# Kernel tuning notes

Hardware: AMD Instinct MI355X
Metric: run time of the kernel (lower is better)

## Reference

```python
import jax, jax.numpy as jnp
import numpy as np

# ---- Hash-grid configuration (matches init_kwargs / torch-ngp HashEncoder) ----
L = 16            # num_levels
D = 2             # level_dim
BASE = 16         # base_resolution
DESIRED = 2048    # desired_resolution
MAXP = 2 ** 19    # 2**log2_hashmap_size
DIVIDE = 1.5

S = np.exp2(np.log2(DESIRED / BASE) / (L - 1))          # per-level scale ~1.3819
RES = np.ceil(BASE * S ** np.arange(L)).astype(np.int64)  # [L] grid resolutions
_sizes = np.minimum(MAXP, (RES + 1) ** 3)
SIZES = (np.ceil(_sizes / 8) * 8).astype(np.int64)       # aligned to 8, per torch-ngp
OFFSETS = np.concatenate([[0], np.cumsum(SIZES)[:-1]])
TOTAL = int(SIZES.sum())  # 6119864
DENSE = (RES + 1) ** 3 <= SIZES                          # levels small enough for direct index
PRIMES = (1, 2654435761, 805459861)


def hash_encode(x01, table):
    """x01: [N,3] in [0,1]; table: [TOTAL, D]. Returns [N, L*D]."""
    N = x01.shape[0]
    scale = jnp.asarray(BASE * S ** np.arange(L) - 1.0, jnp.float32)   # [L]
    pos = x01[:, None, :] * scale[None, :, None] + 0.5                 # [N,L,3]
    pg_f = jnp.floor(pos)
    frac = pos - pg_f                                                  # [N,L,3]
    pg = pg_f.astype(jnp.uint32)

    res1 = jnp.asarray(RES + 1, jnp.uint32)        # [L]
    sizes = jnp.asarray(SIZES, jnp.uint32)         # [L]
    offs = jnp.asarray(OFFSETS, jnp.int32)         # [L]
    dense = jnp.asarray(DENSE)                     # [L] bool

    feat = jnp.zeros((N, L, D), x01.dtype)
    for c in range(8):  # 8 trilinear corners (fixed small loop)
        bit = np.array([(c >> 0) & 1, (c >> 1) & 1, (c >> 2) & 1])
        cg = pg + jnp.asarray(bit, jnp.uint32)                         # [N,L,3]
        w = jnp.prod(jnp.where(jnp.asarray(bit.astype(bool)), frac, 1.0 - frac), axis=-1)  # [N,L]
        idx_dense = cg[..., 0] + cg[..., 1] * res1 + cg[..., 2] * res1 * res1
        h = (cg[..., 0] * jnp.uint32(PRIMES[0])) ^ (cg[..., 1] * jnp.uint32(PRIMES[1])) ^ (cg[..., 2] * jnp.uint32(PRIMES[2]))
        idx = jnp.where(dense[None, :], idx_dense % sizes, h % sizes)  # [N,L]
        gidx = idx.astype(jnp.int32) + offs[None, :]                   # global table index
        feat = feat + w[..., None] * table[gidx]                       # gather + lerp accumulate
    return feat.reshape(N, L * D)


def setup_inputs() -> dict:
    key = jax.random.key(0)
    ks = jax.random.split(key, 10)
    N = 524288
    x = jax.random.uniform(ks[0], (N, 3), jnp.float32)                # coords in [0,1)
    table = jax.random.uniform(ks[1], (TOTAL, D), jnp.float32, -1e-4, 1e-4)
    def lin(k, fi, fo):
        return jax.random.normal(k, (fi, fo), jnp.float32) / np.sqrt(fi)
    return {
        'x': x, 'table': table,
        'w1': lin(ks[2], 32, 256), 'b1': jnp.zeros((256,), jnp.float32),
        'w2': lin(ks[3], 256, 256), 'b2': jnp.zeros((256,), jnp.float32),
        'w3': lin(ks[4], 256, 256), 'b3': jnp.zeros((256,), jnp.float32),
        'w4': lin(ks[5], 256, 3), 'b4': jnp.zeros((3,), jnp.float32),
    }


def reference(x, table, w1, b1, w2, b2, w3, b3, w4, b4):
    feat = hash_encode(x / DIVIDE, table)                 # [N,32]
    h = jax.nn.relu(feat @ w1 + b1)
    h = jax.nn.relu(h @ w2 + b2)
    h = jax.nn.relu(h @ w3 + b3)
    rgb = jax.nn.sigmoid(h @ w4 + b4)                     # [N,3]
    return rgb
```

## Files before the change

kernel.cpp:

```cpp
#include <hip/hip_runtime.h>
#include <hip/hip_bf16.h>
#include <math.h>

#define NTHREADS 256
#define BR 64

typedef __attribute__((ext_vector_type(8))) short   s16x8;
typedef __attribute__((ext_vector_type(8))) __bf16  bf16x8;
typedef __attribute__((ext_vector_type(4))) float   f32x4;
typedef __attribute__((ext_vector_type(2))) float   f32x2;

__device__ __constant__ float c_scale[16] = {
    15.0f,        21.110607f,  29.554930f,  41.224254f,
    57.350239f,   79.634946f,  110.430473f, 152.987205f,
    211.796890f,  293.066769f, 405.374657f, 560.574388f,
    775.046906f,  1071.429232f, 1481.003616f, 2047.0f
};
__device__ __constant__ unsigned c_off[16] = {
    0u,        4920u,     18744u,    51512u,
    136696u,   352696u,   876984u,   1401272u,
    1925560u,  2449848u,  2974136u,  3498424u,
    4022712u,  4547000u,  5071288u,  5595576u
};
__device__ __constant__ unsigned c_res1[16] = {
    17u, 24u, 32u, 44u, 60u, 0u,0u,0u,0u,0u,0u,0u,0u,0u,0u,0u
};

#define TBL_SCALE     8192.0f
#define TBL_SCALE_INV (1.0f/8192.0f)

__device__ inline unsigned short f2bf(float f) {
    unsigned u = __builtin_bit_cast(unsigned, f);
    u += 0x7FFFu + ((u >> 16) & 1u);
    return (unsigned short)(u >> 16);
}
__device__ inline float bf2f(unsigned short h) {
    unsigned u = ((unsigned)h) << 16;
    return __builtin_bit_cast(float, u);
}
__device__ inline unsigned cvtpk(float lo, float hi) {
    unsigned r;
    asm("v_cvt_pk_bf16_f32 %0, %1, %2" : "=v"(r) : "v"(lo), "v"(hi));
    return r;
}
__device__ inline f32x4 mfma_bf16(s16x8 a, s16x8 b, f32x4 c) {
    return __builtin_amdgcn_mfma_f32_16x16x32_bf16(
        __builtin_bit_cast(bf16x8, a), __builtin_bit_cast(bf16x8, b), c, 0, 0, 0);
}

__global__ void convert_w(const float* __restrict__ w1, const float* __restrict__ w2,
                          const float* __restrict__ w3, const float* __restrict__ w4,
                          unsigned short* __restrict__ ws) {
    int t = blockIdx.x * blockDim.x + threadIdx.x;
    if (t < 8192) {
        int col = t >> 5, k = t & 31;
        ws[t] = f2bf(w1[k * 256 + col]);
    } else if (t < 73728) {
        int u = t - 8192; int col = u >> 8, k = u & 255;
        ws[t] = f2bf(w2[k * 256 + col]);
    } else if (t < 139264) {
        int u = t - 73728; int col = u >> 8, k = u & 255;
        ws[t] = f2bf(w3[k * 256 + col]);
    } else if (t < 143360) {
        int u = t - 139264; int ch = u >> 8, k = u & 255;
        ws[t] = (ch < 3) ? f2bf(w4[k * 3 + ch]) : (unsigned short)0;
    }
}

__global__ void convert_table_fp8(const float* __restrict__ t, unsigned short* __restrict__ o, int n) {
    int i = blockIdx.x * blockDim.x + threadIdx.x;
    if (i < n) {
        const float2 v = ((const float2*)t)[i];
        const int pk = __builtin_amdgcn_cvt_pk_fp8_f32(v.x * TBL_SCALE, v.y * TBL_SCALE, 0, false);
        o[i] = (unsigned short)(pk & 0xFFFF);
    }
}

__global__ __launch_bounds__(256)
void encode_kernel(const float* __restrict__ x, const unsigned short* __restrict__ tbf8,
                   uint2* __restrict__ feat2, int N)
{
    const int p  = blockIdx.x * 256 + threadIdx.x;
    const int lp = blockIdx.y;
    if (p >= N) return;

    const float inv = (1.0f / 1.5f);
    const float xc = x[3 * p + 0] * inv;
    const float yc = x[3 * p + 1] * inv;
    const float zc = x[3 * p + 2] * inv;

    unsigned idxa[2][8];
    float rxa[2], rya[2], rza[2];
    #pragma unroll
    for (int s = 0; s < 2; ++s) {
        const int l = lp * 2 + s;
        const float sc = c_scale[l];
        const float px = xc * sc + 0.5f;
        const float py = yc * sc + 0.5f;
        const float pz = zc * sc + 0.5f;
        const float fx = floorf(px), fy = floorf(py), fz = floorf(pz);
        rxa[s] = px - fx; rya[s] = py - fy; rza[s] = pz - fz;
        const unsigned ux = (unsigned)fx, uy = (unsigned)fy, uz = (unsigned)fz;
        const unsigned off = c_off[l];
        const unsigned r1  = c_res1[l];
        const bool dense = (l < 5);
        #pragma unroll
        for (int c = 0; c < 8; ++c) {
            const unsigned cx = ux + (c & 1), cy = uy + ((c >> 1) & 1), cz = uz + ((c >> 2) & 1);
            unsigned idx;
            if (dense) idx = cx + cy * r1 + cz * r1 * r1;
            else       idx = (cx ^ (cy * 2654435761u) ^ (cz * 805459861u)) & 524287u;
            idxa[s][c] = idx + off;
        }
    }

    unsigned short va[2][8];
    #pragma unroll
    for (int s = 0; s < 2; ++s)
        #pragma unroll
        for (int c = 0; c < 8; ++c)
            va[s][c] = tbf8[idxa[s][c]];

    unsigned outv[2];
    #pragma unroll
    for (int s = 0; s < 2; ++s) {
        float ax = 0.0f, ay = 0.0f;
        #pragma unroll
        for (int c = 0; c < 8; ++c) {
            const float wx = (c & 1) ? rxa[s] : (1.0f - rxa[s]);
            const float wy = ((c >> 1) & 1) ? rya[s] : (1.0f - rya[s]);
            const float wz = ((c >> 2) & 1) ? rza[s] : (1.0f - rza[s]);
            const float w = wx * wy * wz;
            const f32x2 tv = __builtin_amdgcn_cvt_pk_f32_fp8((int)va[s][c], false);
            ax = fmaf(w, tv[0], ax);
            ay = fmaf(w, tv[1], ay);
        }
        outv[s] = cvtpk(ax * TBL_SCALE_INV, ay * TBL_SCALE_INV);
    }
    feat2[(size_t)lp * N + p] = make_uint2(outv[0], outv[1]);
}

__global__ __launch_bounds__(NTHREADS, 3)
void mlp_kernel(const uint2* __restrict__ feat2,
                const unsigned short* __restrict__ wt,
                const float* __restrict__ b1, const float* __restrict__ b2,
                const float* __restrict__ b3, const float* __restrict__ b4,
                float* __restrict__ out, int N)
{
    __shared__ unsigned short sA[BR * 256];
    char* sAb = (char*)sA;

    const int tid = threadIdx.x;
    const int p0  = blockIdx.x * BR;
    if (p0 >= N) return;

    #pragma unroll
    for (int it = 0; it < 2; ++it) {
        const int t  = it * NTHREADS + tid;
        const int lp = t >> 6;
        const int p  = t & 63;
        const uint2 v = feat2[(size_t)lp * N + p0 + p];
        *reinterpret_cast<uint2*>(
            sAb + p * 512 + (((unsigned)(lp * 8)) ^ ((unsigned)((p & 7) << 4)))) = v;
    }
    __syncthreads();

    const int lane = tid & 63;
    const int wid  = tid >> 6;
    const int rowb = wid * 64;
    const int arow = lane & 15;
    const int kgrp = lane >> 4;
    const int bcol = lane & 15;

    f32x4 acc[4][4];

    auto epilogue = [&](const float* __restrict__ bias) {
        #pragma unroll
        for (int rt = 0; rt < 4; ++rt) {
            const int f0 = rowb + rt * 16 + kgrp * 4;
            const float4 bv = *reinterpret_cast<const float4*>(bias + f0);
            #pragma unroll
            for (int ct = 0; ct < 4; ++ct) {
                const int p = ct * 16 + bcol;
                const float v0 = fmaxf(acc[rt][ct][0] + bv.x, 0.0f);
                const float v1 = fmaxf(acc[rt][ct][1] + bv.y, 0.0f);
                const float v2 = fmaxf(acc[rt][ct][2] + bv.z, 0.0f);
                const float v3 = fmaxf(acc[rt][ct][3] + bv.w, 0.0f);
                uint2 pk;
                pk.x = cvtpk(v0, v1);
                pk.y = cvtpk(v2, v3);
                *reinterpret_cast<uint2*>(
                    sAb + p * 512 + (((unsigned)(2 * f0)) ^ ((unsigned)((p & 7) << 4)))) = pk;
            }
        }
    };

    {
        #pragma unroll
        for (int rt = 0; rt < 4; ++rt)
            #pragma unroll
            for (int ct = 0; ct < 4; ++ct) acc[rt][ct] = f32x4{0.f, 0.f, 0.f, 0.f};

        s16x8 wfr[4];
        #pragma unroll
        for (int rt = 0; rt < 4; ++rt)
            wfr[rt] = *reinterpret_cast<const s16x8*>(wt + (rowb + rt * 16 + arow) * 32 + kgrp * 8);
        #pragma unroll
        for (int ct = 0; ct < 4; ++ct) {
            const int p = ct * 16 + bcol;
            const s16x8 bfr = *reinterpret_cast<const s16x8*>(
                sAb + p * 512 + (((unsigned)(kgrp * 16)) ^ ((unsigned)((p & 7) << 4))));
            #pragma unroll
            for (int rt = 0; rt < 4; ++rt)
                acc[rt][ct] = mfma_bf16(wfr[rt], bfr, acc[rt][ct]);
        }
        __syncthreads();
        epilogue(b1);
        __syncthreads();
    }

    #pragma unroll 1
    for (int layer = 0; layer < 2; ++layer) {
        const unsigned short* __restrict__ W = wt + 8192 + (layer << 16);
        #pragma unroll
        for (int rt = 0; rt < 4; ++rt)
            #pragma unroll
            for (int ct = 0; ct < 4; ++ct) acc[rt][ct] = f32x4{0.f, 0.f, 0.f, 0.f};

        for (int ks = 0; ks < 8; ++ks) {
            s16x8 wfr[4];
            #pragma unroll
            for (int rt = 0; rt < 4; ++rt)
                wfr[rt] = *reinterpret_cast<const s16x8*>(
                    W + (rowb + rt * 16 + arow) * 256 + ks * 32 + kgrp * 8);
            #pragma unroll
            for (int ct = 0; ct < 4; ++ct) {
                const int p = ct * 16 + bcol;
                const s16x8 bfr = *reinterpret_cast<const s16x8*>(
                    sAb + p * 512 + (((unsigned)(ks * 64 + kgrp * 16)) ^ ((unsigned)((p & 7) << 4))));
                #pragma unroll
                for (int rt = 0; rt < 4; ++rt)
                    acc[rt][ct] = mfma_bf16(wfr[rt], bfr, acc[rt][ct]);
            }
        }
        __syncthreads();
        epilogue(layer == 0 ? b2 : b3);
        __syncthreads();
    }

    {
        const unsigned short* __restrict__ W4 = wt + 139264;
        const int p = wid * 16 + bcol;
        f32x4 a4 = f32x4{0.f, 0.f, 0.f, 0.f};
        #pragma unroll
        for (int ks = 0; ks < 8; ++ks) {
            const s16x8 wfr = *reinterpret_cast<const s16x8*>(W4 + arow * 256 + ks * 32 + kgrp * 8);
            const s16x8 bfr = *reinterpret_cast<const s16x8*>(
                sAb + p * 512 + (((unsigned)(ks * 64 + kgrp * 16)) ^ ((unsigned)((p & 7) << 4))));
            a4 = mfma_bf16(wfr, bfr, a4);
        }
        if (kgrp == 0) {
            const int pi = p0 + p;
            if (pi < N) {
                #pragma unroll
                for (int c = 0; c < 3; ++c) {
                    const float z = a4[c] + b4[c];
                    out[pi * 3 + c] = 1.0f / (1.0f + expf(-z));
                }
            }
        }
    }
}

__global__ __launch_bounds__(NTHREADS, 3)
void fused_hashmlp(const float* __restrict__ x, const float* __restrict__ table,
                   const unsigned short* __restrict__ wt,
                   const float* __restrict__ b1, const float* __restrict__ b2,
                   const float* __restrict__ b3,
                   const float* __restrict__ w4, const float* __restrict__ b4,
                   float* __restrict__ out, int N)
{
    __shared__ float sX[BR][3];
    __shared__ unsigned short sA[BR * 256];
    const int tid = threadIdx.x;
    const int p0  = blockIdx.x * BR;
    if (p0 >= N) return;
    char* sAb = (char*)sA;

    if (tid < BR * 3) sX[tid / 3][tid % 3] = x[p0 * 3 + tid];
    __syncthreads();

    #pragma unroll
    for (int it = 0; it < 4; ++it) {
        const int task = it * NTHREADS + tid;
        const int l = task >> 6;
        const int p = task & 63;
        const float sc  = c_scale[l];
        const float inv = (1.0f / 1.5f);
        const float px = sX[p][0] * inv * sc + 0.5f;
        const float py = sX[p][1] * inv * sc + 0.5f;
        const float pz = sX[p][2] * inv * sc + 0.5f;
        const float fx = floorf(px), fy = floorf(py), fz = floorf(pz);
        const float rx = px - fx, ry = py - fy, rz = pz - fz;
        const unsigned ux = (unsigned)fx, uy = (unsigned)fy, uz = (unsigned)fz;
        const unsigned off = c_off[l];
        const unsigned r1  = c_res1[l];
        const bool dense = (l < 5);
        float ax = 0.0f, ay = 0.0f;
        #pragma unroll
        for (int c = 0; c < 8; ++c) {
            const unsigned bx = c & 1, by = (c >> 1) & 1, bz = (c >> 2) & 1;
            const unsigned cx = ux + bx, cy = uy + by, cz = uz + bz;
            const float wx = bx ? rx : (1.0f - rx);
            const float wy = by ? ry : (1.0f - ry);
            const float wz = bz ? rz : (1.0f - rz);
            const float w = wx * wy * wz;
            unsigned idx;
            if (dense) idx = cx + cy * r1 + cz * r1 * r1;
            else       idx = (cx ^ (cy * 2654435761u) ^ (cz * 805459861u)) & 524287u;
            const float2 tv = *reinterpret_cast<const float2*>(table + 2u * (idx + off));
            ax = fmaf(w, tv.x, ax);
            ay = fmaf(w, tv.y, ay);
        }
        const unsigned pack = (unsigned)f2bf(ax) | ((unsigned)f2bf(ay) << 16);
        *reinterpret_cast<unsigned*>(sAb + p * 512 + ((l * 4) ^ ((p & 7) << 4))) = pack;
    }
    __syncthreads();

    const int lane = tid & 63;
    const int wid  = tid >> 6;
    const int rowb = wid * 64;
    const int arow = lane & 15;
    const int kgrp = lane >> 4;
    const int bcol = lane & 15;

    f32x4 acc[4][4];

    auto epilogue = [&](const float* __restrict__ bias) {
        #pragma unroll
        for (int rt = 0; rt < 4; ++rt) {
            const int f0 = rowb + rt * 16 + kgrp * 4;
            const float4 bv = *reinterpret_cast<const float4*>(bias + f0);
            #pragma unroll
            for (int ct = 0; ct < 4; ++ct) {
                const int p = ct * 16 + bcol;
                const float v0 = fmaxf(acc[rt][ct][0] + bv.x, 0.0f);
                const float v1 = fmaxf(acc[rt][ct][1] + bv.y, 0.0f);
                const float v2 = fmaxf(acc[rt][ct][2] + bv.z, 0.0f);
                const float v3 = fmaxf(acc[rt][ct][3] + bv.w, 0.0f);
                uint2 pk;
                pk.x = (unsigned)f2bf(v0) | ((unsigned)f2bf(v1) << 16);
                pk.y = (unsigned)f2bf(v2) | ((unsigned)f2bf(v3) << 16);
                *reinterpret_cast<uint2*>(
                    sAb + p * 512 + (((unsigned)(2 * f0)) ^ ((unsigned)((p & 7) << 4)))) = pk;
            }
        }
    };

    {
        #pragma unroll
        for (int rt = 0; rt < 4; ++rt)
            #pragma unroll
            for (int ct = 0; ct < 4; ++ct) acc[rt][ct] = f32x4{0.f, 0.f, 0.f, 0.f};
        s16x8 wfr[4];
        #pragma unroll
        for (int rt = 0; rt < 4; ++rt)
            wfr[rt] = *reinterpret_cast<const s16x8*>(wt + (rowb + rt * 16 + arow) * 32 + kgrp * 8);
        #pragma unroll
        for (int ct = 0; ct < 4; ++ct) {
            const int p = ct * 16 + bcol;
            const s16x8 bfr = *reinterpret_cast<const s16x8*>(
                sAb + p * 512 + (((unsigned)(kgrp * 16)) ^ ((unsigned)((p & 7) << 4))));
            #pragma unroll
            for (int rt = 0; rt < 4; ++rt)
                acc[rt][ct] = mfma_bf16(wfr[rt], bfr, acc[rt][ct]);
        }
        __syncthreads();
        epilogue(b1);
        __syncthreads();
    }

    #pragma unroll 1
    for (int layer = 0; layer < 2; ++layer) {
        const unsigned short* __restrict__ W = wt + 8192 + (layer << 16);
        #pragma unroll
        for (int rt = 0; rt < 4; ++rt)
            #pragma unroll
            for (int ct = 0; ct < 4; ++ct) acc[rt][ct] = f32x4{0.f, 0.f, 0.f, 0.f};
        for (int ks = 0; ks < 8; ++ks) {
            s16x8 wfr[4];
            #pragma unroll
            for (int rt = 0; rt < 4; ++rt)
                wfr[rt] = *reinterpret_cast<const s16x8*>(
                    W + (rowb + rt * 16 + arow) * 256 + ks * 32 + kgrp * 8);
            #pragma unroll
            for (int ct = 0; ct < 4; ++ct) {
                const int p = ct * 16 + bcol;
                const s16x8 bfr = *reinterpret_cast<const s16x8*>(
                    sAb + p * 512 + (((unsigned)(ks * 64 + kgrp * 16)) ^ ((unsigned)((p & 7) << 4))));
                #pragma unroll
                for (int rt = 0; rt < 4; ++rt)
                    acc[rt][ct] = mfma_bf16(wfr[rt], bfr, acc[rt][ct]);
            }
        }
        __syncthreads();
        epilogue(layer == 0 ? b2 : b3);
        __syncthreads();
    }

    if (tid < BR * 3) {
        const int r = tid / 3;
        const int c = tid - 3 * r;
        float z0 = 0.0f, z1 = 0.0f;
        for (int kb = 0; kb < 32; kb += 2) {
            const s16x8 hv0 = *reinterpret_cast<const s16x8*>(
                sAb + r * 512 + (((unsigned)(kb * 16)) ^ ((unsigned)((r & 7) << 4))));
            const s16x8 hv1 = *reinterpret_cast<const s16x8*>(
                sAb + r * 512 + (((unsigned)((kb + 1) * 16)) ^ ((unsigned)((r & 7) << 4))));
            #pragma unroll
            for (int j = 0; j < 8; ++j) {
                z0 = fmaf(bf2f((unsigned short)hv0[j]), w4[(kb * 8 + j) * 3 + c], z0);
                z1 = fmaf(bf2f((unsigned short)hv1[j]), w4[((kb + 1) * 8 + j) * 3 + c], z1);
            }
        }
        const float z = z0 + z1 + b4[c];
        const int pi = p0 + r;
        if (pi < N) out[pi * 3 + c] = 1.0f / (1.0f + expf(-z));
    }
}

extern "C" void kernel_launch(void* const* d_in, const int* in_sizes, int n_in,
                              void* d_out, int out_size, void* d_ws, size_t ws_size,
                              hipStream_t stream) {
    const float* x     = (const float*)d_in[0];
    const float* table = (const float*)d_in[1];
    const float* w1    = (const float*)d_in[2];
    const float* b1    = (const float*)d_in[3];
    const float* w2    = (const float*)d_in[4];
    const float* b2    = (const float*)d_in[5];
    const float* w3    = (const float*)d_in[6];
    const float* b3    = (const float*)d_in[7];
    const float* w4    = (const float*)d_in[8];
    const float* b4    = (const float*)d_in[9];
    float* out = (float*)d_out;

    const int N = in_sizes[0] / 3;

    const size_t W_ELEMS    = 143360;
    const size_t TOTAL_E    = 6119864;
    const size_t wt_bytes   = W_ELEMS * 2;
    const size_t tbl_bytes  = TOTAL_E * 2;
    const size_t need_bf    = wt_bytes + tbl_bytes;
    const size_t FEAT_BYTES = (size_t)N * 64;
    const size_t need_split = need_bf + FEAT_BYTES;

    unsigned short* wsw  = (unsigned short*)d_ws;
    unsigned short* tbf8 = (unsigned short*)((char*)d_ws + wt_bytes);
    uint2* feat2 = (uint2*)((char*)d_ws + need_bf);

    hipLaunchKernelGGL(convert_w, dim3(560), dim3(256), 0, stream, w1, w2, w3, w4, wsw);

    if (ws_size >= need_split) {
        hipLaunchKernelGGL(convert_table_fp8, dim3((unsigned)((TOTAL_E + 255) / 256)), dim3(256),
                           0, stream, table, tbf8, (int)TOTAL_E);
        hipLaunchKernelGGL(encode_kernel, dim3((N + 255) / 256, 8), dim3(256), 0, stream,
                           x, tbf8, feat2, N);
        hipLaunchKernelGGL(mlp_kernel, dim3((N + BR - 1) / BR), dim3(NTHREADS), 0, stream,
                           feat2, wsw, b1, b2, b3, b4, out, N);
    } else {
        hipLaunchKernelGGL(fused_hashmlp, dim3((N + BR - 1) / BR), dim3(NTHREADS), 0, stream,
                           x, table, wsw, b1, b2, b3, w4, b4, out, N);
    }
}
```

Baseline: 558.9 us.

## Merge x-adjacent hash-grid corner gathers and widen MLP blocks to 128 rows

The encode kernel now pairs the two x-neighbour corners of each trilinear cell. When their table indices fall in the same aligned 32-bit word, both come from a single 4-byte load; otherwise it falls back to a separate 2-byte gather for the second corner. Dense levels and hashed levels with an even x coordinate qualify, so this should cut the number of random memory transactions. The MLP kernel moves from 256 threads and 64 rows per block to 512 threads and 128 rows, with pairs of waves sharing weight rows. That doubles LDS per block to 64 KB, which may limit how many blocks fit on a CU.

```diff
diff --git a/kernel.cpp b/kernel.cpp
--- a/kernel.cpp
+++ b/kernel.cpp
@@ -4,6 +4,8 @@
 
 #define NTHREADS 256
 #define BR 64
+#define MTHREADS 512
+#define MBR 128
 
 typedef __attribute__((ext_vector_type(8))) short   s16x8;
 typedef __attribute__((ext_vector_type(8))) __bf16  bf16x8;
@@ -89,7 +91,7 @@
     const float yc = x[3 * p + 1] * inv;
     const float zc = x[3 * p + 2] * inv;
 
-    unsigned idxa[2][8];
+    unsigned i0a[2][4], i1a[2][4];
     float rxa[2], rya[2], rza[2];
     #pragma unroll
     for (int s = 0; s < 2; ++s) {
@@ -105,69 +107,95 @@
         const unsigned r1  = c_res1[l];
         const bool dense = (l < 5);
         #pragma unroll
-        for (int c = 0; c < 8; ++c) {
-            const unsigned cx = ux + (c & 1), cy = uy + ((c >> 1) & 1), cz = uz + ((c >> 2) & 1);
-            unsigned idx;
-            if (dense) idx = cx + cy * r1 + cz * r1 * r1;
-            else       idx = (cx ^ (cy * 2654435761u) ^ (cz * 805459861u)) & 524287u;
-            idxa[s][c] = idx + off;
-        }
-    }
-
-    unsigned short va[2][8];
+        for (int j = 0; j < 4; ++j) {
+            const unsigned cy = uy + (j & 1), cz = uz + (j >> 1);
+            unsigned i0, i1;
+            if (dense) {
+                i0 = ux + cy * r1 + cz * r1 * r1;
+                i1 = i0 + 1;
+            } else {
+                const unsigned m = (cy * 2654435761u) ^ (cz * 805459861u);
+                i0 = (ux ^ m) & 524287u;
+                i1 = ((ux + 1u) ^ m) & 524287u;
+            }
+            i0a[s][j] = i0 + off;
+            i1a[s][j] = i1 + off;
+        }
+    }
+
+    unsigned da[2][4];
     #pragma unroll
     for (int s = 0; s < 2; ++s)
         #pragma unroll
-        for (int c = 0; c < 8; ++c)
-            va[s][c] = tbf8[idxa[s][c]];
+        for (int j = 0; j < 4; ++j)
+            da[s][j] = *reinterpret_cast<const unsigned*>(tbf8 + (i0a[s][j] & ~1u));
+
+    unsigned short fb[2][4];
+    #pragma unroll
+    for (int s = 0; s < 2; ++s)
+        #pragma unroll
+        for (int j = 0; j < 4; ++j) {
+            const bool merged = ((i0a[s][j] ^ 1u) == i1a[s][j]);
+            fb[s][j] = merged ? (unsigned short)0 : tbf8[i1a[s][j]];
+        }
 
     unsigned outv[2];
     #pragma unroll
     for (int s = 0; s < 2; ++s) {
         float ax = 0.0f, ay = 0.0f;
         #pragma unroll
-        for (int c = 0; c < 8; ++c) {
-            const float wx = (c & 1) ? rxa[s] : (1.0f - rxa[s]);
-            const float wy = ((c >> 1) & 1) ? rya[s] : (1.0f - rya[s]);
-            const float wz = ((c >> 2) & 1) ? rza[s] : (1.0f - rza[s]);
-            const float w = wx * wy * wz;
-            const f32x2 tv = __builtin_amdgcn_cvt_pk_f32_fp8((int)va[s][c], false);
-            ax = fmaf(w, tv[0], ax);
-            ay = fmaf(w, tv[1], ay);
+        for (int j = 0; j < 4; ++j) {
+            const unsigned i0 = i0a[s][j], i1 = i1a[s][j], d = da[s][j];
+            const unsigned short v0 = (i0 & 1) ? (unsigned short)(d >> 16)
+                                               : (unsigned short)(d & 0xFFFFu);
+            const bool merged = ((i0 ^ 1u) == i1);
+            const unsigned short vm = (i1 & 1) ? (unsigned short)(d >> 16)
+                                               : (unsigned short)(d & 0xFFFFu);
+            const unsigned short v1 = merged ? vm : fb[s][j];
+            const float wy = (j & 1) ? rya[s] : (1.0f - rya[s]);
+            const float wz = (j >> 1) ? rza[s] : (1.0f - rza[s]);
+            const float wyz = wy * wz;
+            const float w0 = (1.0f - rxa[s]) * wyz;
+            const float w1 = rxa[s] * wyz;
+            const f32x2 t0 = __builtin_amdgcn_cvt_pk_f32_fp8((int)v0, false);
+            const f32x2 t1 = __builtin_amdgcn_cvt_pk_f32_fp8((int)v1, false);
+            ax = fmaf(w0, t0[0], ax); ay = fmaf(w0, t0[1], ay);
+            ax = fmaf(w1, t1[0], ax); ay = fmaf(w1, t1[1], ay);
         }
         outv[s] = cvtpk(ax * TBL_SCALE_INV, ay * TBL_SCALE_INV);
     }
     feat2[(size_t)lp * N + p] = make_uint2(outv[0], outv[1]);
 }
 
-__global__ __launch_bounds__(NTHREADS, 3)
+__global__ __launch_bounds__(MTHREADS, 4)
 void mlp_kernel(const uint2* __restrict__ feat2,
                 const unsigned short* __restrict__ wt,
                 const float* __restrict__ b1, const float* __restrict__ b2,
                 const float* __restrict__ b3, const float* __restrict__ b4,
                 float* __restrict__ out, int N)
 {
-    __shared__ unsigned short sA[BR * 256];
+    __shared__ unsigned short sA[MBR * 256];
     char* sAb = (char*)sA;
 
     const int tid = threadIdx.x;
-    const int p0  = blockIdx.x * BR;
+    const int p0  = blockIdx.x * MBR;
     if (p0 >= N) return;
 
     #pragma unroll
     for (int it = 0; it < 2; ++it) {
-        const int t  = it * NTHREADS + tid;
-        const int lp = t >> 6;
-        const int p  = t & 63;
-        const uint2 v = feat2[(size_t)lp * N + p0 + p];
+        const int t  = it * MTHREADS + tid;
+        const int lp = t >> 7;
+        const int pp = t & 127;
+        const uint2 v = feat2[(size_t)lp * N + p0 + pp];
         *reinterpret_cast<uint2*>(
-            sAb + p * 512 + (((unsigned)(lp * 8)) ^ ((unsigned)((p & 7) << 4)))) = v;
+            sAb + pp * 512 + (((unsigned)(lp * 8)) ^ ((unsigned)((pp & 7) << 4)))) = v;
     }
     __syncthreads();
 
     const int lane = tid & 63;
     const int wid  = tid >> 6;
-    const int rowb = wid * 64;
+    const int rowb = (wid & 3) * 64;
+    const int pb   = (wid >> 2) * 64;
     const int arow = lane & 15;
     const int kgrp = lane >> 4;
     const int bcol = lane & 15;
@@ -181,7 +209,7 @@
             const float4 bv = *reinterpret_cast<const float4*>(bias + f0);
             #pragma unroll
             for (int ct = 0; ct < 4; ++ct) {
-                const int p = ct * 16 + bcol;
+                const int pp = pb + ct * 16 + bcol;
                 const float v0 = fmaxf(acc[rt][ct][0] + bv.x, 0.0f);
                 const float v1 = fmaxf(acc[rt][ct][1] + bv.y, 0.0f);
                 const float v2 = fmaxf(acc[rt][ct][2] + bv.z, 0.0f);
@@ -190,7 +218,7 @@
                 pk.x = cvtpk(v0, v1);
                 pk.y = cvtpk(v2, v3);
                 *reinterpret_cast<uint2*>(
-                    sAb + p * 512 + (((unsigned)(2 * f0)) ^ ((unsigned)((p & 7) << 4)))) = pk;
+                    sAb + pp * 512 + (((unsigned)(2 * f0)) ^ ((unsigned)((pp & 7) << 4)))) = pk;
             }
         }
     };
@@ -207,9 +235,9 @@
             wfr[rt] = *reinterpret_cast<const s16x8*>(wt + (rowb + rt * 16 + arow) * 32 + kgrp * 8);
         #pragma unroll
         for (int ct = 0; ct < 4; ++ct) {
-            const int p = ct * 16 + bcol;
+            const int pp = pb + ct * 16 + bcol;
             const s16x8 bfr = *reinterpret_cast<const s16x8*>(
-                sAb + p * 512 + (((unsigned)(kgrp * 16)) ^ ((unsigned)((p & 7) << 4))));
+                sAb + pp * 512 + (((unsigned)(kgrp * 16)) ^ ((unsigned)((pp & 7) << 4))));
             #pragma unroll
             for (int rt = 0; rt < 4; ++rt)
                 acc[rt][ct] = mfma_bf16(wfr[rt], bfr, acc[rt][ct]);
@@ -235,9 +263,9 @@
                     W + (rowb + rt * 16 + arow) * 256 + ks * 32 + kgrp * 8);
             #pragma unroll
             for (int ct = 0; ct < 4; ++ct) {
-                const int p = ct * 16 + bcol;
+                const int pp = pb + ct * 16 + bcol;
                 const s16x8 bfr = *reinterpret_cast<const s16x8*>(
-                    sAb + p * 512 + (((unsigned)(ks * 64 + kgrp * 16)) ^ ((unsigned)((p & 7) << 4))));
+                    sAb + pp * 512 + (((unsigned)(ks * 64 + kgrp * 16)) ^ ((unsigned)((pp & 7) << 4))));
                 #pragma unroll
                 for (int rt = 0; rt < 4; ++rt)
                     acc[rt][ct] = mfma_bf16(wfr[rt], bfr, acc[rt][ct]);
@@ -250,17 +278,17 @@
 
     {
         const unsigned short* __restrict__ W4 = wt + 139264;
-        const int p = wid * 16 + bcol;
+        const int pp = wid * 16 + bcol;
         f32x4 a4 = f32x4{0.f, 0.f, 0.f, 0.f};
         #pragma unroll
         for (int ks = 0; ks < 8; ++ks) {
             const s16x8 wfr = *reinterpret_cast<const s16x8*>(W4 + arow * 256 + ks * 32 + kgrp * 8);
             const s16x8 bfr = *reinterpret_cast<const s16x8*>(
-                sAb + p * 512 + (((unsigned)(ks * 64 + kgrp * 16)) ^ ((unsigned)((p & 7) << 4))));
+                sAb + pp * 512 + (((unsigned)(ks * 64 + kgrp * 16)) ^ ((unsigned)((pp & 7) << 4))));
             a4 = mfma_bf16(wfr, bfr, a4);
         }
         if (kgrp == 0) {
-            const int pi = p0 + p;
+            const int pi = p0 + pp;
             if (pi < N) {
                 #pragma unroll
                 for (int c = 0; c < 3; ++c) {
@@ -465,7 +493,7 @@
                            0, stream, table, tbf8, (int)TOTAL_E);
         hipLaunchKernelGGL(encode_kernel, dim3((N + 255) / 256, 8), dim3(256), 0, stream,
                            x, tbf8, feat2, N);
-        hipLaunchKernelGGL(mlp_kernel, dim3((N + BR - 1) / BR), dim3(NTHREADS), 0, stream,
+        hipLaunchKernelGGL(mlp_kernel, dim3((N + MBR - 1) / MBR), dim3(MTHREADS), 0, stream,
                            feat2, wsw, b1, b2, b3, b4, out, N);
     } else {
         hipLaunchKernelGGL(fused_hashmlp, dim3((N + BR - 1) / BR), dim3(NTHREADS), 0, stream,
```

Result: no change. 563.9 us (+0.9%).
